# Kernel optimization log

Hardware: AMD Instinct MI355X
Metric: run time of the kernel (lower is better)

Reference implementation:

```python
import jax, jax.numpy as jnp
import numpy as np

B, S, D, H, L, K = 16, 384, 512, 8, 4, 7
HD = D // H
MAXLEN = 400


def _pos_encoding(d=D, max_len=MAXLEN):
    # Faithful to the (unusual) torch loop: even idx i -> sin(pos/10000**(2i/d)),
    # odd idx i+1 -> cos(pos/10000**(2(i+1)/d))
    pe = np.zeros((max_len, d), dtype=np.float32)
    pos = np.arange(max_len, dtype=np.float64)[:, None]
    i = np.arange(0, d, 2)
    pe[:, i] = np.sin(pos / 10000.0 ** (2 * i / d))
    pe[:, i + 1] = np.cos(pos / 10000.0 ** (2 * (i + 1) / d))
    return jnp.asarray(pe)

POS_ENC = _pos_encoding()


def layer_norm(x, g, b, eps=1e-5):
    m = jnp.mean(x, -1, keepdims=True)
    v = jnp.mean((x - m) ** 2, -1, keepdims=True)
    return (x - m) * jax.lax.rsqrt(v + eps) * g + b


def dsconv(x, dw_w, pw_w, pw_b):
    # x: [B,S,D]; depthwise conv1d (no bias) then pointwise 1x1 (bias)
    xc = jnp.transpose(x, (0, 2, 1))  # [B,D,S]
    y = jax.lax.conv_general_dilated(
        xc, dw_w, window_strides=(1,), padding=[(K // 2, K // 2)],
        dimension_numbers=("NCH", "OIH", "NCH"), feature_group_count=D)  # [B,D,S]
    return jnp.einsum("bcs,oc->bso", y, pw_w) + pw_b  # [B,S,D]


def setup_inputs():
    key = jax.random.key(0)
    ks = jax.random.split(key, 16)
    sc = 0.02
    inp = {
        "x": jax.random.normal(ks[0], (B, S, D), jnp.float32),
        "mask": jax.random.randint(ks[1], (B, S), 0, 2, jnp.int32),
        "dw_w": jax.random.normal(ks[2], (L, D, 1, K), jnp.float32) * sc,
        "pw_w": jax.random.normal(ks[3], (L, D, D), jnp.float32) * sc,
        "pw_b": jnp.zeros((L, D), jnp.float32),
        "conv_ln_g": jnp.ones((L, D), jnp.float32),
        "conv_ln_b": jnp.zeros((L, D), jnp.float32),
        "pos_ln_g": jnp.ones((D,), jnp.float32),
        "pos_ln_b": jnp.zeros((D,), jnp.float32),
        "wq": jax.random.normal(ks[4], (D, D), jnp.float32) * sc,
        "bq": jnp.zeros((D,), jnp.float32),
        "wk": jax.random.normal(ks[5], (D, D), jnp.float32) * sc,
        "bk": jnp.zeros((D,), jnp.float32),
        "wv": jax.random.normal(ks[6], (D, D), jnp.float32) * sc,
        "bv": jnp.zeros((D,), jnp.float32),
        "wo": jax.random.normal(ks[7], (D, D), jnp.float32) * sc,
        "bo": jnp.zeros((D,), jnp.float32),
        "ff_ln_g": jnp.ones((D,), jnp.float32),
        "ff_ln_b": jnp.zeros((D,), jnp.float32),
        "ff_w": jax.random.normal(ks[8], (D, D), jnp.float32) * sc,
        "ff_b": jnp.zeros((D,), jnp.float32),
    }
    return inp


def attention(x, mask, wq, bq, wk, bk, wv, bv, wo, bo):
    def heads(w, b):
        y = jnp.einsum("bsd,od->bso", x, w) + b
        return jnp.transpose(y.reshape(B, S, H, HD), (0, 2, 1, 3))  # [B,H,S,HD]
    q, k, v = heads(wq, bq), heads(wk, bk), heads(wv, bv)
    energy = jnp.einsum("bhqd,bhkd->bhqk", q, k) / jnp.sqrt(jnp.float32(HD))
    m = (mask == 1)[:, None, None, :]  # [B,1,1,S]
    energy = jnp.where(m, jnp.float32(-1e10), energy)
    alpha = jax.nn.softmax(energy, axis=-1)  # dropout = identity (eval)
    a = jnp.einsum("bhqk,bhkd->bhqd", alpha, v)
    a = jnp.transpose(a, (0, 2, 1, 3)).reshape(B, S, D)
    return jnp.einsum("bsd,od->bso", a, wo) + bo


def reference(x, mask, dw_w, pw_w, pw_b, conv_ln_g, conv_ln_b, pos_ln_g, pos_ln_b,
              wq, bq, wk, bk, wv, bv, wo, bo, ff_ln_g, ff_ln_b, ff_w, ff_b):
    out = x + POS_ENC[None, :S, :]
    res = out
    out = layer_norm(out, pos_ln_g, pos_ln_b)
    for i in range(L):
        out = jax.nn.relu(dsconv(out, dw_w[i], pw_w[i], pw_b[i]))
        out = out + res  # dropout = identity (eval)
        res = out
        out = layer_norm(out, conv_ln_g[i], conv_ln_b[i])
    out = attention(out, mask, wq, bq, wk, bk, wv, bv, wo, bo)
    out = out + res
    res = out
    out = layer_norm(out, ff_ln_g, ff_ln_b)
    out = jax.nn.relu(jnp.einsum("bsd,od->bso", out, ff_w) + ff_b)
    return out + res
```

## Files before the change

kernel.cpp:

```cpp
#include <hip/hip_runtime.h>

#define BB 16
#define SS 384
#define DD 512
#define HH 8
#define HDIM 64
#define LLAY 4
#define KW 7
#define MM (BB*SS)

typedef unsigned short u16;
typedef unsigned int u32;
typedef short short8v __attribute__((ext_vector_type(8)));
typedef float floatx4 __attribute__((ext_vector_type(4)));

__device__ __forceinline__ float bf2f(u16 u) {
    union { u32 i; float f; } v; v.i = ((u32)u) << 16; return v.f;
}
__device__ __forceinline__ u16 f2bf(float f) {
    union { float f; u32 i; } v; v.f = f;
    return (u16)((v.i + 0x7FFFu + ((v.i >> 16) & 1u)) >> 16);
}
__device__ __forceinline__ bool sniff_f32(const void* dtp) {
    return *((const u32*)dtp) == 0x3F800000u;
}
__device__ __forceinline__ float ldf(const void* p, long i, bool f32) {
    return f32 ? ((const float*)p)[i] : bf2f(((const u16*)p)[i]);
}
__device__ __forceinline__ short8v ldfrag_scalar(const void* p, long i, bool f32) {
    short8v r;
    if (f32) {
        const float* q = (const float*)p + i;
#pragma unroll
        for (int j = 0; j < 8; j++) r[j] = (short)f2bf(q[j]);
    } else {
        r = *(const short8v*)((const u16*)p + i);
    }
    return r;
}

__device__ __forceinline__ void load_lds16(const u16* g, u16* l) {
    __builtin_amdgcn_global_load_lds((const __attribute__((address_space(1))) void*)g,
                                     (__attribute__((address_space(3))) void*)l, 16, 0, 0);
}
__device__ __forceinline__ int swz(int row) { return (row & 3) ^ ((row >> 2) & 3); }
__device__ __forceinline__ short8v lds_frag(const u16* buf, int row, int quad) {
    return *(const short8v*)(buf + ((size_t)row * 4 + (quad ^ swz(row))) * 8);
}

__device__ __forceinline__ floatx4 mfma16(short8v a, short8v b, floatx4 c) {
    return __builtin_amdgcn_mfma_f32_16x16x32_bf16(a, b, c, 0, 0, 0);
}

#define WCV_DW 2359296
#define WCV_TOT (WCV_DW + LLAY*KW*DD)
#define NCVB ((WCV_TOT + 255) / 256)

__global__ __launch_bounds__(256) void posln_cvt_kernel(
    const void* __restrict__ x, const void* __restrict__ g, const void* __restrict__ bvec,
    u16* __restrict__ res, u16* __restrict__ out,
    const void* __restrict__ pw_w, const void* __restrict__ wq,
    const void* __restrict__ wk, const void* __restrict__ wv,
    const void* __restrict__ wo, const void* __restrict__ ff_w,
    const void* __restrict__ dw_w, u16* __restrict__ wdst,
    const void* __restrict__ dtp) {
    const bool f32 = sniff_f32(dtp);
    const int tid = threadIdx.x;
    if (blockIdx.x >= MM) {
        const int i = (blockIdx.x - MM) * 256 + tid;
        if (i >= WCV_TOT) return;
        const void* src; long idx;
        if (i < 1048576) { src = pw_w; idx = i; }
        else if (i < WCV_DW) {
            const int j = i - 1048576;
            const int m = j >> 18;
            idx = j & 262143;
            src = (m == 0) ? wq : (m == 1) ? wk : (m == 2) ? wv : (m == 3) ? wo : ff_w;
        } else {
            const int j = i - WCV_DW;
            const int l = j / (KW * DD);
            const int r1 = j % (KW * DD);
            const int t = r1 / DD, c = r1 % DD;
            src = dw_w; idx = ((long)l * DD + c) * KW + t;
        }
        wdst[i] = f2bf(ldf(src, idx, f32));
        return;
    }
    const int row = blockIdx.x;
    const int s = row % SS;
    float v[2];
#pragma unroll
    for (int i = 0; i < 2; i++) {
        const int d = tid + i * 256;
        const float freq = __expf(-(float)d * 0.035977892078032f);
        const float arg = (float)s * freq;
        const float pe = (d & 1) ? __cosf(arg) : __sinf(arg);
        v[i] = ldf(x, (long)row * DD + d, f32) + pe;
        res[row * DD + d] = f2bf(v[i]);
    }
    float sum = v[0] + v[1], sq = v[0] * v[0] + v[1] * v[1];
#pragma unroll
    for (int off = 32; off; off >>= 1) { sum += __shfl_down(sum, off); sq += __shfl_down(sq, off); }
    __shared__ float red[4][2];
    const int wv2 = tid >> 6;
    if ((tid & 63) == 0) { red[wv2][0] = sum; red[wv2][1] = sq; }
    __syncthreads();
    sum = red[0][0] + red[1][0] + red[2][0] + red[3][0];
    sq  = red[0][1] + red[1][1] + red[2][1] + red[3][1];
    const float mean = sum * (1.f / DD);
    const float rstd = rsqrtf(sq * (1.f / DD) - mean * mean + 1e-5f);
#pragma unroll
    for (int i = 0; i < 2; i++) {
        const int d = tid + i * 256;
        out[row * DD + d] = f2bf((v[i] - mean) * rstd * ldf(g, d, f32) + ldf(bvec, d, f32));
    }
}

__global__ __launch_bounds__(512) void lnres_kernel(const u16* __restrict__ y,
                                                    const void* __restrict__ g,
                                                    const void* __restrict__ bvec,
                                                    int blayer,
                                                    u16* __restrict__ out,
                                                    const void* __restrict__ dtp) {
    const bool f32 = sniff_f32(dtp);
    const long voff = (long)blayer * DD;
    const int row = blockIdx.x * 8 + (threadIdx.x >> 6);
    const int lane = threadIdx.x & 63;
    const short8v v = *(const short8v*)(y + (size_t)row * DD + lane * 8);
    float f[8], sum = 0.f, sq = 0.f;
#pragma unroll
    for (int j = 0; j < 8; j++) { f[j] = bf2f((u16)v[j]); sum += f[j]; sq += f[j] * f[j]; }
#pragma unroll
    for (int off = 32; off; off >>= 1) { sum += __shfl_xor(sum, off); sq += __shfl_xor(sq, off); }
    const float mean = sum * (1.f / DD);
    const float rstd = rsqrtf(sq * (1.f / DD) - mean * mean + 1e-5f);
    short8v o;
#pragma unroll
    for (int j = 0; j < 8; j++) {
        const int d = lane * 8 + j;
        o[j] = (short)f2bf((f[j] - mean) * rstd * ldf(g, voff + d, f32) + ldf(bvec, voff + d, f32));
    }
    *(short8v*)(out + (size_t)row * DD + lane * 8) = o;
}

__global__ __launch_bounds__(256) void dwln_kernel(
    const u16* __restrict__ res, const u16* __restrict__ wdw ,
    const void* __restrict__ g, const void* __restrict__ bvec, int voff,
    u16* __restrict__ out, const void* __restrict__ dtp) {
    const bool f32 = sniff_f32(dtp);
    __shared__ __align__(16) u16 rows[14][DD];
    const int tid = threadIdx.x;
    const int lane = tid & 63, wave = tid >> 6;
    const int m0 = blockIdx.x * 8;
#pragma unroll
    for (int j = 0; j < 4; j++) {
        const int c = j * 256 + tid;
        if (c < 896) {
            int gr = m0 - 3 + (c >> 6);
            gr = (gr < 0) ? 0 : (gr >= MM ? MM - 1 : gr);
            load_lds16(res + (size_t)gr * DD + (c & 63) * 8, &rows[0][0] + (size_t)c * 8);
        }
    }
    float gv[8], bv[8];
#pragma unroll
    for (int e = 0; e < 8; e++) {
        gv[e] = ldf(g, (long)voff + lane * 8 + e, f32);
        bv[e] = ldf(bvec, (long)voff + lane * 8 + e, f32);
    }
    asm volatile("s_waitcnt vmcnt(0)\n\ts_barrier" ::: "memory");
    for (int j = wave; j < 14; j += 4) {
        const short8v v = *(const short8v*)&rows[j][lane * 8];
        float f[8], s = 0.f, q = 0.f;
#pragma unroll
        for (int e = 0; e < 8; e++) { f[e] = bf2f((u16)v[e]); s += f[e]; q += f[e] * f[e]; }
#pragma unroll
        for (int off = 32; off; off >>= 1) { s += __shfl_xor(s, off); q += __shfl_xor(q, off); }
        const float mean = s * (1.f / DD);
        const float rstd = rsqrtf(q * (1.f / DD) - mean * mean + 1e-5f);
        short8v o;
#pragma unroll
        for (int e = 0; e < 8; e++) o[e] = (short)f2bf((f[e] - mean) * rstd * gv[e] + bv[e]);
        *(short8v*)&rows[j][lane * 8] = o;
    }
    asm volatile("s_waitcnt lgkmcnt(0)\n\ts_barrier" ::: "memory");
    short8v wv[KW];
#pragma unroll
    for (int t = 0; t < KW; t++) wv[t] = *(const short8v*)(wdw + t * DD + lane * 8);
#pragma unroll
    for (int rr = wave; rr < 8; rr += 4) {
        const int gm = m0 + rr, s = gm % SS;
        float acc[8] = {0, 0, 0, 0, 0, 0, 0, 0};
#pragma unroll
        for (int t = 0; t < KW; t++) {
            const int ss2 = s + t - 3;
            if (ss2 >= 0 && ss2 < SS) {
                const short8v iv = *(const short8v*)&rows[rr + t][lane * 8];
#pragma unroll
                for (int e = 0; e < 8; e++) acc[e] += bf2f((u16)iv[e]) * bf2f((u16)wv[t][e]);
            }
        }
        short8v ov;
#pragma unroll
        for (int e = 0; e < 8; e++) ov[e] = (short)f2bf(acc[e]);
        *(short8v*)(out + (size_t)gm * DD + lane * 8) = ov;
    }
}

__global__ __launch_bounds__(256) void dwconv_kernel(const u16* __restrict__ in,
                                                     const void* __restrict__ w, int layer,
                                                     u16* __restrict__ out,
                                                     const void* __restrict__ dtp) {
    const bool f32 = sniff_f32(dtp);
    const long woff = (long)layer * DD * KW;
    const int idx = blockIdx.x * 256 + threadIdx.x;
    const int c = idx & (DD - 1);
    const int ms = idx >> 9;
    const int s = ms % SS;
    float acc = 0.f;
#pragma unroll
    for (int t = 0; t < KW; t++) {
        const int ss2 = s + t - 3;
        if (ss2 >= 0 && ss2 < SS)
            acc += bf2f(in[(ms + t - 3) * DD + c]) * ldf(w, woff + c * KW + t, f32);
    }
    out[idx] = f2bf(acc);
}

#define ASTG (64 * 32)
#define WSTG (128 * 32)
__device__ __forceinline__ void stage64(const u16* A, const u16* Wp, int m0,
                                        u16* Ab, u16* Wb, int tid, int k0) {
#pragma unroll
    for (int j = 0; j < 2; j++) {
        const int c = j * 256 + tid;
        const int row = c >> 2;
        const int kp = (c & 3) ^ swz(row);
        load_lds16(Wp + (size_t)row * DD + k0 + kp * 8, Wb + (size_t)c * 8);
    }
    {
        const int row = tid >> 2;
        const int kp = (tid & 3) ^ swz(row);
        load_lds16(A + (size_t)(m0 + row) * DD + k0 + kp * 8, Ab + (size_t)tid * 8);
    }
}

__device__ __forceinline__ void kloop64(const u16* A, const u16* Wp, int m0,
                                        u16* Abuf, u16* Wbuf,
                                        int tid, int wm, int wn, int ln15, int quad,
                                        floatx4 acc[2][4]) {
    stage64(A, Wp, m0, Abuf, Wbuf, tid, 0);
    stage64(A, Wp, m0, Abuf + ASTG, Wbuf + WSTG, tid, 32);
    stage64(A, Wp, m0, Abuf + 2 * ASTG, Wbuf + 2 * WSTG, tid, 64);
#pragma unroll
    for (int ks = 0; ks < 16; ks++) {
        const int cur = ks & 3;
        u16* Ab = Abuf + cur * ASTG;
        u16* Wb = Wbuf + cur * WSTG;
        if (ks < 13) {
            const int nxt = (ks + 3) & 3;
            stage64(A, Wp, m0, Abuf + nxt * ASTG, Wbuf + nxt * WSTG, tid, (ks + 3) * 32);
            asm volatile("s_waitcnt vmcnt(9)\n\ts_barrier" ::: "memory");
        } else if (ks == 13) {
            asm volatile("s_waitcnt vmcnt(6)\n\ts_barrier" ::: "memory");
        } else if (ks == 14) {
            asm volatile("s_waitcnt vmcnt(3)\n\ts_barrier" ::: "memory");
        } else {
            asm volatile("s_waitcnt vmcnt(0)\n\ts_barrier" ::: "memory");
        }
        const short8v a0 = lds_frag(Ab, wm * 32 + ln15, quad);
        const short8v a1 = lds_frag(Ab, wm * 32 + 16 + ln15, quad);
#pragma unroll
        for (int nt = 0; nt < 4; nt++) {
            const short8v b = lds_frag(Wb, wn * 64 + nt * 16 + ln15, quad);
            acc[0][nt] = mfma16(a0, b, acc[0][nt]);
            acc[1][nt] = mfma16(a1, b, acc[1][nt]);
        }
        asm volatile("s_waitcnt lgkmcnt(0)\n\ts_barrier" ::: "memory");
    }
}

template <int RELU, int FINAL>
__global__ __launch_bounds__(256, 2) void gemm64_kernel(
    const u16* __restrict__ A, const u16* __restrict__ W,
    const void* __restrict__ bias, int blayer,
    const u16* __restrict__ res_in, u16* __restrict__ res_out,
    void* __restrict__ out, const void* __restrict__ dtp) {
    const bool f32 = sniff_f32(dtp);
    const long voff = (long)blayer * DD;
    __shared__ __align__(16) u16 smem[4 * (ASTG + WSTG)];
    u16* Wbuf = smem;
    u16* Abuf = smem + 4 * WSTG;
    const int tid = threadIdx.x;
    const int m0 = blockIdx.x * 64, n0 = blockIdx.y * 128;
    const int wave = tid >> 6, lane = tid & 63;
    const int wm = wave >> 1, wn = wave & 1;
    const int ln15 = lane & 15, quad = lane >> 4;

    floatx4 acc[2][4];
#pragma unroll
    for (int mt = 0; mt < 2; mt++)
#pragma unroll
        for (int nt = 0; nt < 4; nt++) acc[mt][nt] = {0.f, 0.f, 0.f, 0.f};

    kloop64(A, W + (size_t)n0 * DD, m0, Abuf, Wbuf, tid, wm, wn, ln15, quad, acc);

#pragma unroll
    for (int nt = 0; nt < 4; nt++) {
        const int col = n0 + wn * 64 + nt * 16 + ln15;
        const float bval = ldf(bias, voff + col, f32);
#pragma unroll
        for (int mt = 0; mt < 2; mt++)
#pragma unroll
            for (int r = 0; r < 4; r++) {
                const int m = m0 + wm * 32 + mt * 16 + quad * 4 + r;
                float y = acc[mt][nt][r] + bval;
                if (RELU) y = fmaxf(y, 0.f);
                y += bf2f(res_in[(size_t)m * DD + col]);
                if (res_out) res_out[(size_t)m * DD + col] = f2bf(y);
                if constexpr (FINAL) {
                    if (f32) ((float*)out)[(size_t)m * DD + col] = y;
                    else     ((u16*)out)[(size_t)m * DD + col] = f2bf(y);
                }
            }
    }
}

#define VP 72
__global__ __launch_bounds__(256, 2) void qkv64_kernel(
    const u16* __restrict__ A,
    const u16* __restrict__ Wq, const u16* __restrict__ Wk, const u16* __restrict__ Wv,
    const void* __restrict__ bq, const void* __restrict__ bk, const void* __restrict__ bv,
    u16* __restrict__ qo, u16* __restrict__ ko, u16* __restrict__ vo,
    const void* __restrict__ dtp) {
    const bool f32 = sniff_f32(dtp);
    const int sel = blockIdx.z;
    const u16* W = (sel == 0) ? Wq : (sel == 1) ? Wk : Wv;
    const void* bias = (sel == 0) ? bq : (sel == 1) ? bk : bv;

    __shared__ __align__(16) u16 smem[4 * (ASTG + WSTG)];
    u16* Wbuf = smem;
    u16* Abuf = smem + 4 * WSTG;
    u16 (*vtile)[VP] = (u16 (*)[VP])smem;

    const int tid = threadIdx.x;
    const int m0 = blockIdx.x * 64, n0 = blockIdx.y * 128;
    const int wave = tid >> 6, lane = tid & 63;
    const int wm = wave >> 1, wn = wave & 1;
    const int ln15 = lane & 15, quad = lane >> 4;
    const int bidx = m0 / SS;

    floatx4 acc[2][4];
#pragma unroll
    for (int mt = 0; mt < 2; mt++)
#pragma unroll
        for (int nt = 0; nt < 4; nt++) acc[mt][nt] = {0.f, 0.f, 0.f, 0.f};

    kloop64(A, W + (size_t)n0 * DD, m0, Abuf, Wbuf, tid, wm, wn, ln15, quad, acc);

    if (sel == 2) {
#pragma unroll
        for (int nt = 0; nt < 4; nt++) {
            const int cl = wn * 64 + nt * 16 + ln15;
            const float bval = ldf(bias, n0 + cl, f32);
#pragma unroll
            for (int mt = 0; mt < 2; mt++)
#pragma unroll
                for (int r = 0; r < 4; r++)
                    vtile[cl][wm * 32 + mt * 16 + quad * 4 + r] = f2bf(acc[mt][nt][r] + bval);
        }
        __syncthreads();
        const int c = tid & 127, half = tid >> 7;
        const int col = n0 + c;
        const int h = col >> 6, hd = col & 63;
        u16* dst = vo + ((size_t)(bidx * HH + h) * HDIM + hd) * SS
                      + (m0 - bidx * SS) + half * 32;
        const u16* srcl = &vtile[c][half * 32];
#pragma unroll
        for (int j = 0; j < 4; j++)
            *(short8v*)(dst + j * 8) = *(const short8v*)(srcl + j * 8);
    } else {
        u16* out = (sel == 0) ? qo : ko;
#pragma unroll
        for (int nt = 0; nt < 4; nt++) {
            const int col = n0 + wn * 64 + nt * 16 + ln15;
            const int h = col >> 6, hd = col & 63;
            const float bval = ldf(bias, col, f32);
#pragma unroll
            for (int mt = 0; mt < 2; mt++)
#pragma unroll
                for (int r = 0; r < 4; r++) {
                    const int m = m0 + wm * 32 + mt * 16 + quad * 4 + r;
                    const int s = m - bidx * SS;
                    out[((size_t)(bidx * HH + h) * SS + s) * HDIM + hd] = f2bf(acc[mt][nt][r] + bval);
                }
        }
    }
}

template <int RELU, int DO_LN, int FINAL>
__global__ __launch_bounds__(512, 4) void gemm16_kernel(
    const u16* __restrict__ A, const void* __restrict__ W, int wlayer,
    const void* __restrict__ bias, const void* __restrict__ g,
    const void* __restrict__ bvec, int blayer,
    const u16* __restrict__ res_in, u16* __restrict__ res_out,
    void* __restrict__ out, const void* __restrict__ dtp) {
    const bool f32 = sniff_f32(dtp);
    const long woff = (long)wlayer * DD * DD;
    const long voff = (long)blayer * DD;
    __shared__ float part[8][16][2];
    const int tid = threadIdx.x;
    const int m0 = blockIdx.x * 16;
    const int wave = tid >> 6, lane = tid & 63;
    const int ln15 = lane & 15, quad = lane >> 4;

    floatx4 acc[4];
#pragma unroll
    for (int nt = 0; nt < 4; nt++) acc[nt] = {0.f, 0.f, 0.f, 0.f};

    const u16* A0 = A + (size_t)(m0 + ln15) * DD + quad * 8;
#pragma unroll
    for (int ks = 0; ks < 16; ks++) {
        const int k0 = ks * 32;
        short8v a0 = *(const short8v*)(A0 + k0);
        short8v b[4];
#pragma unroll
        for (int nt = 0; nt < 4; nt++) {
            const long wrow = woff + (long)(wave * 64 + nt * 16 + ln15) * DD + quad * 8 + k0;
            b[nt] = ldfrag_scalar(W, wrow, f32);
        }
#pragma unroll
        for (int nt = 0; nt < 4; nt++)
            acc[nt] = mfma16(a0, b[nt], acc[nt]);
    }

#pragma unroll
    for (int nt = 0; nt < 4; nt++) {
        const int col = wave * 64 + nt * 16 + ln15;
        const float bval = ldf(bias, voff + col, f32);
#pragma unroll
        for (int r = 0; r < 4; r++) {
            const int m = m0 + quad * 4 + r;
            float y = acc[nt][r] + bval;
            if (RELU) y = fmaxf(y, 0.f);
            y += bf2f(res_in[(size_t)m * DD + col]);
            if (res_out) res_out[(size_t)m * DD + col] = f2bf(y);
            acc[nt][r] = y;
        }
    }
    if constexpr (DO_LN) {
        float ls[4], lq[4];
#pragma unroll
        for (int r = 0; r < 4; r++) {
            float s = 0.f, q = 0.f;
#pragma unroll
            for (int nt = 0; nt < 4; nt++) { const float y = acc[nt][r]; s += y; q += y * y; }
            ls[r] = s; lq[r] = q;
        }
#pragma unroll
        for (int off = 1; off < 16; off <<= 1)
#pragma unroll
            for (int r = 0; r < 4; r++) {
                ls[r] += __shfl_xor(ls[r], off);
                lq[r] += __shfl_xor(lq[r], off);
            }
        if (ln15 == 0) {
#pragma unroll
            for (int r = 0; r < 4; r++) {
                part[wave][quad * 4 + r][0] = ls[r];
                part[wave][quad * 4 + r][1] = lq[r];
            }
        }
        __syncthreads();
        float mean[4], rstd[4];
#pragma unroll
        for (int r = 0; r < 4; r++) {
            const int rr = quad * 4 + r;
            float s = 0.f, q = 0.f;
#pragma unroll
            for (int wv = 0; wv < 8; wv++) { s += part[wv][rr][0]; q += part[wv][rr][1]; }
            const float mn = s * (1.f / DD);
            mean[r] = mn;
            rstd[r] = rsqrtf(q * (1.f / DD) - mn * mn + 1e-5f);
        }
#pragma unroll
        for (int nt = 0; nt < 4; nt++) {
            const int col = wave * 64 + nt * 16 + ln15;
            const float gv = ldf(g, voff + col, f32);
            const float bv = ldf(bvec, voff + col, f32);
#pragma unroll
            for (int r = 0; r < 4; r++) {
                const int m = m0 + quad * 4 + r;
                ((u16*)out)[(size_t)m * DD + col] =
                    f2bf((acc[nt][r] - mean[r]) * rstd[r] * gv + bv);
            }
        }
    } else {
#pragma unroll
        for (int nt = 0; nt < 4; nt++) {
            const int col = wave * 64 + nt * 16 + ln15;
#pragma unroll
            for (int r = 0; r < 4; r++) {
                const int m = m0 + quad * 4 + r;
                if (FINAL && f32) ((float*)out)[(size_t)m * DD + col] = acc[nt][r];
                else              ((u16*)out)[(size_t)m * DD + col] = f2bf(acc[nt][r]);
            }
        }
    }
}

__global__ __launch_bounds__(512, 4) void qkv16_kernel(
    const u16* __restrict__ A,
    const void* __restrict__ Wq, const void* __restrict__ Wk, const void* __restrict__ Wv,
    const void* __restrict__ bq, const void* __restrict__ bk, const void* __restrict__ bv,
    u16* __restrict__ qo, u16* __restrict__ ko, u16* __restrict__ vo,
    const void* __restrict__ dtp) {
    const bool f32 = sniff_f32(dtp);
    const int sel = blockIdx.y;
    const void* W = (sel == 0) ? Wq : (sel == 1) ? Wk : Wv;
    const void* bias = (sel == 0) ? bq : (sel == 1) ? bk : bv;

    const int tid = threadIdx.x;
    const int m0 = blockIdx.x * 16;
    const int wave = tid >> 6, lane = tid & 63;
    const int ln15 = lane & 15, quad = lane >> 4;
    const int bidx = m0 / SS;

    floatx4 acc[4];
#pragma unroll
    for (int nt = 0; nt < 4; nt++) acc[nt] = {0.f, 0.f, 0.f, 0.f};

    const u16* A0 = A + (size_t)(m0 + ln15) * DD + quad * 8;
#pragma unroll
    for (int ks = 0; ks < 16; ks++) {
        const int k0 = ks * 32;
        short8v a0 = *(const short8v*)(A0 + k0);
        short8v b[4];
#pragma unroll
        for (int nt = 0; nt < 4; nt++) {
            const long wrow = (long)(wave * 64 + nt * 16 + ln15) * DD + quad * 8 + k0;
            b[nt] = ldfrag_scalar(W, wrow, f32);
        }
#pragma unroll
        for (int nt = 0; nt < 4; nt++)
            acc[nt] = mfma16(a0, b[nt], acc[nt]);
    }

    if (sel == 2) {
#pragma unroll
        for (int nt = 0; nt < 4; nt++) {
            const int col = wave * 64 + nt * 16 + ln15;
            const int h = col >> 6, hd = col & 63;
            const float bval = ldf(bias, col, f32);
#pragma unroll
            for (int r = 0; r < 4; r++) {
                const int m = m0 + quad * 4 + r;
                const int s = m - bidx * SS;
                vo[((size_t)(bidx * HH + h) * HDIM + hd) * SS + s] = f2bf(acc[nt][r] + bval);
            }
        }
    } else {
        u16* out = (sel == 0) ? qo : ko;
#pragma unroll
        for (int nt = 0; nt < 4; nt++) {
            const int col = wave * 64 + nt * 16 + ln15;
            const int h = col >> 6, hd = col & 63;
            const float bval = ldf(bias, col, f32);
#pragma unroll
            for (int r = 0; r < 4; r++) {
                const int m = m0 + quad * 4 + r;
                const int s = m - bidx * SS;
                out[((size_t)(bidx * HH + h) * SS + s) * HDIM + hd] = f2bf(acc[nt][r] + bval);
            }
        }
    }
}

#define ALP 392
__global__ __launch_bounds__(256) void attn_kernel(const u16* __restrict__ q,
                                                   const u16* __restrict__ k,
                                                   const u16* __restrict__ vT,
                                                   const int* __restrict__ mask,
                                                   u16* __restrict__ out) {
    __shared__ __align__(16) u16 Kb[3072 * 8];
    __shared__ __align__(16) u16 Vb[3072 * 8];
    __shared__ __align__(16) u16 al4[4][16][ALP];

    const int n = blockIdx.x;
    const int i = n >> 3;
    const int g = (n & 7) * 16 + i / 6;
    const int sub = i % 6;
    const int h = g & 7, b = g >> 3;
    const int tid = threadIdx.x;
    const int wave = tid >> 6, lane = tid & 63;
    const int ln15 = lane & 15, quad = lane >> 4;
    const int q0 = (sub * 4 + wave) * 16;

    const u16* qh = q + (size_t)(b * HH + h) * SS * HDIM;
    const u16* kh = k + (size_t)(b * HH + h) * SS * HDIM;
    const u16* vh = vT + (size_t)(b * HH + h) * HDIM * SS;

#pragma unroll
    for (int j = 0; j < 12; j++) {
        const int c = j * 256 + tid;
        const int row = c >> 3, cc = c & 7;
        const int kp = cc ^ ((row ^ (row >> 3)) & 7);
        load_lds16(kh + (size_t)row * HDIM + kp * 8, Kb + (size_t)c * 8);
    }
#pragma unroll
    for (int j = 0; j < 12; j++) {
        const int c = j * 256 + tid;
        const int tile = c >> 8, rr = (c >> 2) & 63, cc = c & 3;
        const int kp = cc ^ swz(rr);
        load_lds16(vh + (size_t)rr * SS + tile * 32 + kp * 8, Vb + (size_t)c * 8);
    }
    const short8v* arow = (const short8v*)(qh + (q0 + ln15) * HDIM + quad * 8);
    const short8v a0 = arow[0], a1 = arow[4];
    __syncthreads();

    floatx4 sc[24];
#pragma unroll
    for (int t = 0; t < 24; t++) {
        const int row = t * 16 + ln15;
        const int s3 = (row ^ (row >> 3)) & 7;
        const short8v b0 = *(const short8v*)(Kb + ((size_t)row * 8 + (quad ^ s3)) * 8);
        const short8v b1 = *(const short8v*)(Kb + ((size_t)row * 8 + ((4 + quad) ^ s3)) * 8);
        floatx4 acc = {0.f, 0.f, 0.f, 0.f};
        acc = mfma16(a0, b0, acc);
        acc = mfma16(a1, b1, acc);
        sc[t] = acc;
    }
    float mx[4] = {-3.0e38f, -3.0e38f, -3.0e38f, -3.0e38f};
#pragma unroll
    for (int t = 0; t < 24; t++) {
        const bool msk = (mask[b * SS + t * 16 + ln15] == 1);
#pragma unroll
        for (int r = 0; r < 4; r++) {
            float v = sc[t][r] * 0.125f;
            if (msk) v = -1e10f;
            sc[t][r] = v;
            mx[r] = fmaxf(mx[r], v);
        }
    }
#pragma unroll
    for (int off = 8; off; off >>= 1)
#pragma unroll
        for (int r = 0; r < 4; r++) mx[r] = fmaxf(mx[r], __shfl_xor(mx[r], off, 16));
    float sum[4] = {0.f, 0.f, 0.f, 0.f};
    u16* alw = &al4[wave][0][0];
#pragma unroll
    for (int t = 0; t < 24; t++) {
#pragma unroll
        for (int r = 0; r < 4; r++) {
            const float p = __expf(sc[t][r] - mx[r]);
            sum[r] += p;
            alw[(quad * 4 + r) * ALP + t * 16 + ln15] = f2bf(p);
        }
    }
#pragma unroll
    for (int off = 8; off; off >>= 1)
#pragma unroll
        for (int r = 0; r < 4; r++) sum[r] += __shfl_xor(sum[r], off, 16);
    __builtin_amdgcn_s_waitcnt(0);

#pragma unroll
    for (int dt = 0; dt < 4; dt++) {
        floatx4 acc = {0.f, 0.f, 0.f, 0.f};
        const int row = dt * 16 + ln15;
        const int vsw = quad ^ swz(row);
#pragma unroll
        for (int c2 = 0; c2 < 12; c2++) {
            const short8v af = *(const short8v*)(alw + ln15 * ALP + c2 * 32 + quad * 8);
            const short8v bf = *(const short8v*)(Vb + ((size_t)c2 * 256 + row * 4 + vsw) * 8);
            acc = mfma16(af, bf, acc);
        }
#pragma unroll
        for (int rr = 0; rr < 4; rr++) {
            const int s = q0 + quad * 4 + rr;
            out[((size_t)(b * SS + s)) * DD + h * HDIM + dt * 16 + ln15] = f2bf(acc[rr] / sum[rr]);
        }
    }
}

extern "C" void kernel_launch(void* const* d_in, const int* in_sizes, int n_in,
                              void* d_out, int out_size, void* d_ws, size_t ws_size,
                              hipStream_t stream) {
    (void)in_sizes; (void)n_in; (void)out_size;
    const void* x     = d_in[0];
    const int*  mask  = (const int*)d_in[1];
    const void* dw_w  = d_in[2];
    const void* pw_w  = d_in[3];
    const void* pw_b  = d_in[4];
    const void* cln_g = d_in[5];
    const void* cln_b = d_in[6];
    const void* pln_g = d_in[7];
    const void* pln_b = d_in[8];
    const void* wq    = d_in[9];
    const void* bq    = d_in[10];
    const void* wk    = d_in[11];
    const void* bk    = d_in[12];
    const void* wv    = d_in[13];
    const void* bv    = d_in[14];
    const void* wo    = d_in[15];
    const void* bo    = d_in[16];
    const void* fln_g = d_in[17];
    const void* fln_b = d_in[18];
    const void* ff_w  = d_in[19];
    const void* ff_b  = d_in[20];
    const void* dtp   = cln_g;

    const size_t nAct = (size_t)MM * DD;
    char* p = (char*)d_ws;
    u16* res   = (u16*)p; p += nAct * 2;
    u16* lnout = (u16*)p; p += nAct * 2;
    u16* tmp   = (u16*)p; p += nAct * 2;
    u16* vT    = (u16*)p; p += nAct * 2;
    u16* wcv   = (u16*)p;
    u16* kb    = (u16*)d_out;

    const size_t needFast = nAct * 2 * 4 + (size_t)WCV_TOT * 2;
    const bool fast = (ws_size >= needFast);

    if (fast) {
        posln_cvt_kernel<<<MM + NCVB, 256, 0, stream>>>(
            x, pln_g, pln_b, res, lnout,
            pw_w, wq, wk, wv, wo, ff_w, dw_w, wcv, dtp);
        const u16* w_pw = wcv;
        const u16* w_q  = wcv + 1048576;
        const u16* w_k  = wcv + 1310720;
        const u16* w_v  = wcv + 1572864;
        const u16* w_o  = wcv + 1835008;
        const u16* w_ff = wcv + 2097152;
        const u16* w_dw = wcv + WCV_DW;

        for (int i = 0; i < LLAY; i++) {
            const void* lg = (i == 0) ? pln_g : cln_g;
            const void* lb = (i == 0) ? pln_b : cln_b;
            const int lo = (i == 0) ? 0 : (i - 1) * DD;
            dwln_kernel<<<MM / 8, 256, 0, stream>>>(
                res, w_dw + (size_t)i * KW * DD, lg, lb, lo, tmp, dtp);
            gemm64_kernel<1, 0><<<dim3(MM / 64, 4), 256, 0, stream>>>(
                tmp, w_pw + (size_t)i * DD * DD, pw_b, i, res, res, nullptr, dtp);
        }
        lnres_kernel<<<MM / 8, 512, 0, stream>>>(res, cln_g, cln_b, LLAY - 1, lnout, dtp);
        qkv64_kernel<<<dim3(MM / 64, 4, 3), 256, 0, stream>>>(
            lnout, w_q, w_k, w_v, bq, bk, bv, tmp, kb, vT, dtp);

        attn_kernel<<<BB * HH * (SS / 64), 256, 0, stream>>>(tmp, kb, vT, mask, lnout);

        gemm64_kernel<0, 0><<<dim3(MM / 64, 4), 256, 0, stream>>>(
            lnout, w_o, bo, 0, res, res, nullptr, dtp);
        lnres_kernel<<<MM / 8, 512, 0, stream>>>(res, fln_g, fln_b, 0, lnout, dtp);
        gemm64_kernel<1, 1><<<dim3(MM / 64, 4), 256, 0, stream>>>(
            lnout, w_ff, ff_b, 0, res, nullptr, d_out, dtp);
    } else {
        posln_cvt_kernel<<<MM, 256, 0, stream>>>(
            x, pln_g, pln_b, res, lnout,
            pw_w, wq, wk, wv, wo, ff_w, dw_w, (u16*)d_ws, dtp);
        for (int i = 0; i < LLAY; i++) {
            dwconv_kernel<<<MM * DD / 256, 256, 0, stream>>>(lnout, dw_w, i, tmp, dtp);
            gemm16_kernel<1, 1, 0><<<MM / 16, 512, 0, stream>>>(
                tmp, pw_w, i, pw_b, cln_g, cln_b, i, res, res, lnout, dtp);
        }
        qkv16_kernel<<<dim3(MM / 16, 3), 512, 0, stream>>>(
            lnout, wq, wk, wv, bq, bk, bv, tmp, kb, vT, dtp);

        attn_kernel<<<BB * HH * (SS / 64), 256, 0, stream>>>(tmp, kb, vT, mask, lnout);

        gemm16_kernel<0, 1, 0><<<MM / 16, 512, 0, stream>>>(
            lnout, wo, 0, bo, fln_g, fln_b, 0, res, res, lnout, dtp);
        gemm16_kernel<1, 0, 1><<<MM / 16, 512, 0, stream>>>(
            lnout, ff_w, 0, ff_b, nullptr, nullptr, 0, res, nullptr, d_out, dtp);
    }
}
```

Measured before the change: 321.5 us.

## Fold pre-GEMM LayerNorms into weights and epilogues using atomically accumulated row stats

Removes the two standalone LayerNorm kernels before the QKV and FF GEMMs. The producing GEMMs now accumulate per-row sum and sum-of-squares with atomics. The gamma scaling is folded into the bf16 weights, and the mean and beta corrections go into the consuming GEMM epilogue through precomputed u/v vectors. This saves two full activation passes and launches. In exchange it adds atomics, a one-pass variance formula on unnormalized bf16 inputs (a numerical risk), and extra setup blocks in the conversion kernel.

```diff
diff --git a/kernel.cpp b/kernel.cpp
--- a/kernel.cpp
+++ b/kernel.cpp
@@ -55,6 +55,9 @@
 #define WCV_DW 2359296
 #define WCV_TOT (WCV_DW + LLAY*KW*DD)
 #define NCVB ((WCV_TOT + 255) / 256)
+#define NUVB 512
+#define NZB  96
+#define NSTATS (4 * MM)
 
 __global__ __launch_bounds__(256) void posln_cvt_kernel(
     const void* __restrict__ x, const void* __restrict__ g, const void* __restrict__ bvec,
@@ -63,27 +66,57 @@
     const void* __restrict__ wk, const void* __restrict__ wv,
     const void* __restrict__ wo, const void* __restrict__ ff_w,
     const void* __restrict__ dw_w, u16* __restrict__ wdst,
+    float* __restrict__ uvp, float* __restrict__ statsp,
+    const void* __restrict__ cln_g, const void* __restrict__ cln_b,
+    const void* __restrict__ fln_g, const void* __restrict__ fln_b,
     const void* __restrict__ dtp) {
     const bool f32 = sniff_f32(dtp);
     const int tid = threadIdx.x;
     if (blockIdx.x >= MM) {
-        const int i = (blockIdx.x - MM) * 256 + tid;
-        if (i >= WCV_TOT) return;
-        const void* src; long idx;
-        if (i < 1048576) { src = pw_w; idx = i; }
-        else if (i < WCV_DW) {
-            const int j = i - 1048576;
-            const int m = j >> 18;
-            idx = j & 262143;
-            src = (m == 0) ? wq : (m == 1) ? wk : (m == 2) ? wv : (m == 3) ? wo : ff_w;
+        const int ib = blockIdx.x - MM;
+        if (ib < NCVB) {
+            const int i = ib * 256 + tid;
+            if (i >= WCV_TOT) return;
+            const void* src; long idx; float scale = 1.f;
+            if (i < 1048576) { src = pw_w; idx = i; }
+            else if (i < WCV_DW) {
+                const int j = i - 1048576;
+                const int m = j >> 18;
+                idx = j & 262143;
+                src = (m == 0) ? wq : (m == 1) ? wk : (m == 2) ? wv : (m == 3) ? wo : ff_w;
+                const int k = (int)(idx & 511);
+                if (m <= 2)      scale = ldf(cln_g, 1536 + k, f32);
+                else if (m == 4) scale = ldf(fln_g, k, f32);
+            } else {
+                const int j = i - WCV_DW;
+                const int l = j / (KW * DD);
+                const int r1 = j % (KW * DD);
+                const int t = r1 / DD, c = r1 % DD;
+                src = dw_w; idx = ((long)l * DD + c) * KW + t;
+            }
+            wdst[i] = f2bf(scale * ldf(src, idx, f32));
+        } else if (ib < NCVB + NUVB) {
+            const int i2 = ib - NCVB;
+            const int wave = tid >> 6, lane = tid & 63;
+            const int gn = i2 * 4 + wave;
+            const int mat = gn >> 9, n = gn & 511;
+            const void* srcm = (mat == 0) ? wq : (mat == 1) ? wk : (mat == 2) ? wv : ff_w;
+            float su = 0.f, sv = 0.f;
+#pragma unroll
+            for (int e = 0; e < 8; e++) {
+                const int k = lane * 8 + e;
+                const float w = ldf(srcm, (long)n * 512 + k, f32);
+                const float gg = (mat < 3) ? ldf(cln_g, 1536 + k, f32) : ldf(fln_g, k, f32);
+                const float bb = (mat < 3) ? ldf(cln_b, 1536 + k, f32) : ldf(fln_b, k, f32);
+                su += gg * w; sv += bb * w;
+            }
+#pragma unroll
+            for (int off = 32; off; off >>= 1) { su += __shfl_xor(su, off); sv += __shfl_xor(sv, off); }
+            if (lane == 0) { uvp[mat * 1024 + n] = su; uvp[mat * 1024 + 512 + n] = sv; }
         } else {
-            const int j = i - WCV_DW;
-            const int l = j / (KW * DD);
-            const int r1 = j % (KW * DD);
-            const int t = r1 / DD, c = r1 % DD;
-            src = dw_w; idx = ((long)l * DD + c) * KW + t;
-        }
-        wdst[i] = f2bf(ldf(src, idx, f32));
+            const int idx = (ib - NCVB - NUVB) * 256 + tid;
+            if (idx < NSTATS) statsp[idx] = 0.f;
+        }
         return;
     }
     const int row = blockIdx.x;
@@ -98,6 +131,7 @@
         v[i] = ldf(x, (long)row * DD + d, f32) + pe;
         res[row * DD + d] = f2bf(v[i]);
     }
+    if (out == nullptr) return;
     float sum = v[0] + v[1], sq = v[0] * v[0] + v[1] * v[1];
 #pragma unroll
     for (int off = 32; off; off >>= 1) { sum += __shfl_down(sum, off); sq += __shfl_down(sq, off); }
@@ -114,33 +148,6 @@
         const int d = tid + i * 256;
         out[row * DD + d] = f2bf((v[i] - mean) * rstd * ldf(g, d, f32) + ldf(bvec, d, f32));
     }
-}
-
-__global__ __launch_bounds__(512) void lnres_kernel(const u16* __restrict__ y,
-                                                    const void* __restrict__ g,
-                                                    const void* __restrict__ bvec,
-                                                    int blayer,
-                                                    u16* __restrict__ out,
-                                                    const void* __restrict__ dtp) {
-    const bool f32 = sniff_f32(dtp);
-    const long voff = (long)blayer * DD;
-    const int row = blockIdx.x * 8 + (threadIdx.x >> 6);
-    const int lane = threadIdx.x & 63;
-    const short8v v = *(const short8v*)(y + (size_t)row * DD + lane * 8);
-    float f[8], sum = 0.f, sq = 0.f;
-#pragma unroll
-    for (int j = 0; j < 8; j++) { f[j] = bf2f((u16)v[j]); sum += f[j]; sq += f[j] * f[j]; }
-#pragma unroll
-    for (int off = 32; off; off >>= 1) { sum += __shfl_xor(sum, off); sq += __shfl_xor(sq, off); }
-    const float mean = sum * (1.f / DD);
-    const float rstd = rsqrtf(sq * (1.f / DD) - mean * mean + 1e-5f);
-    short8v o;
-#pragma unroll
-    for (int j = 0; j < 8; j++) {
-        const int d = lane * 8 + j;
-        o[j] = (short)f2bf((f[j] - mean) * rstd * ldf(g, voff + d, f32) + ldf(bvec, voff + d, f32));
-    }
-    *(short8v*)(out + (size_t)row * DD + lane * 8) = o;
 }
 
 __global__ __launch_bounds__(256) void dwln_kernel(
@@ -279,12 +286,16 @@
     }
 }
 
-template <int RELU, int FINAL>
+template <int RELU, int FINAL, int STATS, int LNF>
 __global__ __launch_bounds__(256, 2) void gemm64_kernel(
     const u16* __restrict__ A, const u16* __restrict__ W,
     const void* __restrict__ bias, int blayer,
     const u16* __restrict__ res_in, u16* __restrict__ res_out,
-    void* __restrict__ out, const void* __restrict__ dtp) {
+    void* __restrict__ out,
+    const float* __restrict__ uvf,
+    const float* __restrict__ sin_sum, const float* __restrict__ sin_sq,
+    float* __restrict__ so_sum, float* __restrict__ so_sq,
+    const void* __restrict__ dtp) {
     const bool f32 = sniff_f32(dtp);
     const long voff = (long)blayer * DD;
     __shared__ __align__(16) u16 smem[4 * (ASTG + WSTG)];
@@ -304,6 +315,26 @@
 
     kloop64(A, W + (size_t)n0 * DD, m0, Abuf, Wbuf, tid, wm, wn, ln15, quad, acc);
 
+    float mu[2][4], rs[2][4];
+    if constexpr (LNF) {
+#pragma unroll
+        for (int mt = 0; mt < 2; mt++)
+#pragma unroll
+            for (int r = 0; r < 4; r++) {
+                const int m = m0 + wm * 32 + mt * 16 + quad * 4 + r;
+                const float s = sin_sum[m] * (1.f / DD);
+                const float q = sin_sq[m] * (1.f / DD);
+                mu[mt][r] = s;
+                rs[mt][r] = rsqrtf(q - s * s + 1e-5f);
+            }
+    }
+    float st[2][4], sq2[2][4];
+    if constexpr (STATS) {
+#pragma unroll
+        for (int mt = 0; mt < 2; mt++)
+#pragma unroll
+            for (int r = 0; r < 4; r++) { st[mt][r] = 0.f; sq2[mt][r] = 0.f; }
+    }
 #pragma unroll
     for (int nt = 0; nt < 4; nt++) {
         const int col = n0 + wn * 64 + nt * 16 + ln15;
@@ -313,7 +344,11 @@
 #pragma unroll
             for (int r = 0; r < 4; r++) {
                 const int m = m0 + wm * 32 + mt * 16 + quad * 4 + r;
-                float y = acc[mt][nt][r] + bval;
+                float y = acc[mt][nt][r];
+                if constexpr (LNF)
+                    y = rs[mt][r] * y - rs[mt][r] * mu[mt][r] * uvf[col] + uvf[512 + col] + bval;
+                else
+                    y += bval;
                 if (RELU) y = fmaxf(y, 0.f);
                 y += bf2f(res_in[(size_t)m * DD + col]);
                 if (res_out) res_out[(size_t)m * DD + col] = f2bf(y);
@@ -321,6 +356,25 @@
                     if (f32) ((float*)out)[(size_t)m * DD + col] = y;
                     else     ((u16*)out)[(size_t)m * DD + col] = f2bf(y);
                 }
+                if constexpr (STATS) { st[mt][r] += y; sq2[mt][r] += y * y; }
+            }
+    }
+    if constexpr (STATS) {
+#pragma unroll
+        for (int mt = 0; mt < 2; mt++)
+#pragma unroll
+            for (int r = 0; r < 4; r++) {
+                float s = st[mt][r], q = sq2[mt][r];
+#pragma unroll
+                for (int off = 1; off < 16; off <<= 1) {
+                    s += __shfl_xor(s, off, 16);
+                    q += __shfl_xor(q, off, 16);
+                }
+                if (ln15 == 0) {
+                    const int m = m0 + wm * 32 + mt * 16 + quad * 4 + r;
+                    atomicAdd(&so_sum[m], s);
+                    atomicAdd(&so_sq[m], q);
+                }
             }
     }
 }
@@ -331,11 +385,14 @@
     const u16* __restrict__ Wq, const u16* __restrict__ Wk, const u16* __restrict__ Wv,
     const void* __restrict__ bq, const void* __restrict__ bk, const void* __restrict__ bv,
     u16* __restrict__ qo, u16* __restrict__ ko, u16* __restrict__ vo,
+    const float* __restrict__ uvp,
+    const float* __restrict__ ssum, const float* __restrict__ ssq,
     const void* __restrict__ dtp) {
     const bool f32 = sniff_f32(dtp);
     const int sel = blockIdx.z;
     const u16* W = (sel == 0) ? Wq : (sel == 1) ? Wk : Wv;
     const void* bias = (sel == 0) ? bq : (sel == 1) ? bk : bv;
+    const float* uvf = uvp + sel * 1024;
 
     __shared__ __align__(16) u16 smem[4 * (ASTG + WSTG)];
     u16* Wbuf = smem;
@@ -357,16 +414,32 @@
 
     kloop64(A, W + (size_t)n0 * DD, m0, Abuf, Wbuf, tid, wm, wn, ln15, quad, acc);
 
+    float mu[2][4], rs[2][4];
+#pragma unroll
+    for (int mt = 0; mt < 2; mt++)
+#pragma unroll
+        for (int r = 0; r < 4; r++) {
+            const int m = m0 + wm * 32 + mt * 16 + quad * 4 + r;
+            const float s = ssum[m] * (1.f / DD);
+            const float q = ssq[m] * (1.f / DD);
+            mu[mt][r] = s;
+            rs[mt][r] = rsqrtf(q - s * s + 1e-5f);
+        }
+
     if (sel == 2) {
 #pragma unroll
         for (int nt = 0; nt < 4; nt++) {
             const int cl = wn * 64 + nt * 16 + ln15;
-            const float bval = ldf(bias, n0 + cl, f32);
+            const int col = n0 + cl;
+            const float bval = ldf(bias, col, f32);
 #pragma unroll
             for (int mt = 0; mt < 2; mt++)
 #pragma unroll
-                for (int r = 0; r < 4; r++)
-                    vtile[cl][wm * 32 + mt * 16 + quad * 4 + r] = f2bf(acc[mt][nt][r] + bval);
+                for (int r = 0; r < 4; r++) {
+                    const float y = rs[mt][r] * acc[mt][nt][r]
+                                  - rs[mt][r] * mu[mt][r] * uvf[col] + uvf[512 + col] + bval;
+                    vtile[cl][wm * 32 + mt * 16 + quad * 4 + r] = f2bf(y);
+                }
         }
         __syncthreads();
         const int c = tid & 127, half = tid >> 7;
@@ -391,7 +464,9 @@
                 for (int r = 0; r < 4; r++) {
                     const int m = m0 + wm * 32 + mt * 16 + quad * 4 + r;
                     const int s = m - bidx * SS;
-                    out[((size_t)(bidx * HH + h) * SS + s) * HDIM + hd] = f2bf(acc[mt][nt][r] + bval);
+                    const float y = rs[mt][r] * acc[mt][nt][r]
+                                  - rs[mt][r] * mu[mt][r] * uvf[col] + uvf[512 + col] + bval;
+                    out[((size_t)(bidx * HH + h) * SS + s) * HDIM + hd] = f2bf(y);
                 }
         }
     }
@@ -714,16 +789,23 @@
     u16* lnout = (u16*)p; p += nAct * 2;
     u16* tmp   = (u16*)p; p += nAct * 2;
     u16* vT    = (u16*)p; p += nAct * 2;
-    u16* wcv   = (u16*)p;
+    u16* wcv   = (u16*)p; p += (size_t)WCV_TOT * 2;
+    float* uvp    = (float*)p; p += 4096 * 4;
+    float* statsp = (float*)p;
+    float* sA_sum = statsp;
+    float* sA_sq  = statsp + MM;
+    float* sB_sum = statsp + 2 * MM;
+    float* sB_sq  = statsp + 3 * MM;
     u16* kb    = (u16*)d_out;
 
-    const size_t needFast = nAct * 2 * 4 + (size_t)WCV_TOT * 2;
+    const size_t needFast = nAct * 2 * 4 + (size_t)WCV_TOT * 2 + (4096 + NSTATS) * 4;
     const bool fast = (ws_size >= needFast);
 
     if (fast) {
-        posln_cvt_kernel<<<MM + NCVB, 256, 0, stream>>>(
-            x, pln_g, pln_b, res, lnout,
-            pw_w, wq, wk, wv, wo, ff_w, dw_w, wcv, dtp);
+        posln_cvt_kernel<<<MM + NCVB + NUVB + NZB, 256, 0, stream>>>(
+            x, pln_g, pln_b, res, nullptr ,
+            pw_w, wq, wk, wv, wo, ff_w, dw_w, wcv, uvp, statsp,
+            cln_g, cln_b, fln_g, fln_b, dtp);
         const u16* w_pw = wcv;
         const u16* w_q  = wcv + 1048576;
         const u16* w_k  = wcv + 1310720;
@@ -732,30 +814,38 @@
         const u16* w_ff = wcv + 2097152;
         const u16* w_dw = wcv + WCV_DW;
 
-        for (int i = 0; i < LLAY; i++) {
+        for (int i = 0; i < LLAY - 1; i++) {
             const void* lg = (i == 0) ? pln_g : cln_g;
             const void* lb = (i == 0) ? pln_b : cln_b;
             const int lo = (i == 0) ? 0 : (i - 1) * DD;
             dwln_kernel<<<MM / 8, 256, 0, stream>>>(
                 res, w_dw + (size_t)i * KW * DD, lg, lb, lo, tmp, dtp);
-            gemm64_kernel<1, 0><<<dim3(MM / 64, 4), 256, 0, stream>>>(
-                tmp, w_pw + (size_t)i * DD * DD, pw_b, i, res, res, nullptr, dtp);
-        }
-        lnres_kernel<<<MM / 8, 512, 0, stream>>>(res, cln_g, cln_b, LLAY - 1, lnout, dtp);
+            gemm64_kernel<1, 0, 0, 0><<<dim3(MM / 64, 4), 256, 0, stream>>>(
+                tmp, w_pw + (size_t)i * DD * DD, pw_b, i, res, res, nullptr,
+                nullptr, nullptr, nullptr, nullptr, nullptr, dtp);
+        }
+        dwln_kernel<<<MM / 8, 256, 0, stream>>>(
+            res, w_dw + (size_t)3 * KW * DD, cln_g, cln_b, 2 * DD, tmp, dtp);
+        gemm64_kernel<1, 0, 1, 0><<<dim3(MM / 64, 4), 256, 0, stream>>>(
+            tmp, w_pw + (size_t)3 * DD * DD, pw_b, 3, res, res, nullptr,
+            nullptr, nullptr, nullptr, sA_sum, sA_sq, dtp);
+
         qkv64_kernel<<<dim3(MM / 64, 4, 3), 256, 0, stream>>>(
-            lnout, w_q, w_k, w_v, bq, bk, bv, tmp, kb, vT, dtp);
+            res, w_q, w_k, w_v, bq, bk, bv, tmp, kb, vT, uvp, sA_sum, sA_sq, dtp);
 
         attn_kernel<<<BB * HH * (SS / 64), 256, 0, stream>>>(tmp, kb, vT, mask, lnout);
 
-        gemm64_kernel<0, 0><<<dim3(MM / 64, 4), 256, 0, stream>>>(
-            lnout, w_o, bo, 0, res, res, nullptr, dtp);
-        lnres_kernel<<<MM / 8, 512, 0, stream>>>(res, fln_g, fln_b, 0, lnout, dtp);
-        gemm64_kernel<1, 1><<<dim3(MM / 64, 4), 256, 0, stream>>>(
-            lnout, w_ff, ff_b, 0, res, nullptr, d_out, dtp);
+        gemm64_kernel<0, 0, 1, 0><<<dim3(MM / 64, 4), 256, 0, stream>>>(
+            lnout, w_o, bo, 0, res, res, nullptr,
+            nullptr, nullptr, nullptr, sB_sum, sB_sq, dtp);
+        gemm64_kernel<1, 1, 0, 1><<<dim3(MM / 64, 4), 256, 0, stream>>>(
+            res, w_ff, ff_b, 0, res, nullptr, d_out,
+            uvp + 3 * 1024, sB_sum, sB_sq, nullptr, nullptr, dtp);
     } else {
         posln_cvt_kernel<<<MM, 256, 0, stream>>>(
             x, pln_g, pln_b, res, lnout,
-            pw_w, wq, wk, wv, wo, ff_w, dw_w, (u16*)d_ws, dtp);
+            pw_w, wq, wk, wv, wo, ff_w, dw_w, (u16*)d_ws, uvp, statsp,
+            cln_g, cln_b, fln_g, fln_b, dtp);
         for (int i = 0; i < LLAY; i++) {
             dwconv_kernel<<<MM * DD / 256, 256, 0, stream>>>(lnout, dw_w, i, tmp, dtp);
             gemm16_kernel<1, 1, 0><<<MM / 16, 512, 0, stream>>>(
```

Measured after the change: 309.5 us, median of 2. -3.7%, faster.
